# Optimization experiments

Hardware: AMD Instinct MI355X
Metric: run time of the kernel (lower is better)

## Reference

```python
import jax, jax.numpy as jnp
import numpy as np

N_TOKENS, MODEL_DIM, NUM_EXPERTS = 65536, 1024, 64
CAPACITY_FACTOR = 1.0


def setup_inputs() -> dict:
    key = jax.random.key(0)
    k1, k2 = jax.random.split(key)
    x = jax.random.normal(k1, (N_TOKENS, MODEL_DIM), dtype=jnp.float32)
    # gate projection weight, torch Linear stores [out_features, in_features]
    wg = jax.random.normal(k2, (NUM_EXPERTS, MODEL_DIM), dtype=jnp.float32) * (1.0 / np.sqrt(MODEL_DIM))
    return {"x": x, "wg": wg}


def reference(x, wg):
    N, E = x.shape[0], wg.shape[0]
    logits = x @ wg.T                              # [N, E]
    # training-branch capacity: capacity_factor * ceil(N / E)
    capacity = int(CAPACITY_FACTOR * ((N + E - 1) // E))
    indices1_s = jnp.argmax(logits, axis=1)        # [N] top-1 expert per token
    gates = jax.nn.softmax(logits, axis=1)         # [N, E]
    mask1 = jax.nn.one_hot(indices1_s, E, dtype=gates.dtype)  # [N, E]
    gates1_s = jnp.sum(gates * mask1, axis=1)      # [N] gate value of chosen expert
    # locations1_s[i] = number of earlier tokens routed to the same expert
    # (exclusive prefix count = inclusive cumsum - 1 at the selected column)
    locations1 = jnp.cumsum(mask1, axis=0) - 1.0   # [N, E]
    locations1_s = jnp.sum(locations1 * mask1, axis=1).astype(jnp.int32)
    # auxiliary load-balance loss (float32 branch of the original)
    me = jnp.sum(gates, axis=0)                    # [E]
    ce = jnp.sum(mask1, axis=0)                    # [E]
    l_aux = jnp.sum(me * ce) * (E / (N * N))
    return (l_aux, indices1_s.astype(jnp.int32), capacity, locations1_s, gates1_s, E)
```

## Files before the change

kernel.cpp:

```cpp
#include <hip/hip_runtime.h>

#define NT 65536
#define MD 1024
#define NE 64
#define TB 128
#define NGATE (NT / TB)
#define NGRP (NT / 64)

typedef short bf16x8 __attribute__((ext_vector_type(8)));
typedef float f32x4  __attribute__((ext_vector_type(4)));

__device__ __forceinline__ void split1(float f, ushort& h, ushort& m, ushort& lo) {
    unsigned u  = __float_as_uint(f);
    unsigned hb = u & 0xFFFF0000u;
    float    r1 = f - __uint_as_float(hb);
    unsigned mb = __float_as_uint(r1) & 0xFFFF0000u;
    float    r2 = r1 - __uint_as_float(mb);
    h  = (ushort)(hb >> 16);
    m  = (ushort)(mb >> 16);
    lo = (ushort)(__float_as_uint(r2) >> 16);
}

__device__ __forceinline__ void split8(const float4 a, const float4 b,
                                       bf16x8& h, bf16x8& m, bf16x8& lo) {
    float f[8] = {a.x, a.y, a.z, a.w, b.x, b.y, b.z, b.w};
#pragma unroll
    for (int j = 0; j < 8; ++j) {
        ushort hh, mm, ll;
        split1(f[j], hh, mm, ll);
        h[j] = (short)hh; m[j] = (short)mm; lo[j] = (short)ll;
    }
}

__global__ __launch_bounds__(256) void prep_kernel(
    const float* __restrict__ wg, ushort* __restrict__ wgp)
{
    const int idx = blockIdx.x * 256 + threadIdx.x;
    const int l  = idx & 63;
    const int nt = (idx >> 6) & 3;
    const int c  = idx >> 8;
    const int e  = nt * 16 + (l & 15);
    const int k0 = c * 32 + (l >> 4) * 8;
    const float* src = wg + (size_t)e * MD + k0;
    float4 a = *(const float4*)(src);
    float4 b = *(const float4*)(src + 4);
    bf16x8 h, m, lo;
    split8(a, b, h, m, lo);
    *(bf16x8*)(wgp + (size_t)idx * 8)          = h;
    *(bf16x8*)(wgp + 65536 + (size_t)idx * 8)  = m;
    *(bf16x8*)(wgp + 131072 + (size_t)idx * 8) = lo;
}

#define MFMA6(accv, xh, xm, xl, wh, wm, wl)                                        \
    accv = __builtin_amdgcn_mfma_f32_16x16x32_bf16(xh, wh, accv, 0, 0, 0);         \
    accv = __builtin_amdgcn_mfma_f32_16x16x32_bf16(xh, wm, accv, 0, 0, 0);         \
    accv = __builtin_amdgcn_mfma_f32_16x16x32_bf16(xm, wh, accv, 0, 0, 0);         \
    accv = __builtin_amdgcn_mfma_f32_16x16x32_bf16(xm, wm, accv, 0, 0, 0);         \
    accv = __builtin_amdgcn_mfma_f32_16x16x32_bf16(xh, wl, accv, 0, 0, 0);         \
    accv = __builtin_amdgcn_mfma_f32_16x16x32_bf16(xl, wh, accv, 0, 0, 0);

__global__ __launch_bounds__(256, 2) void gate_kernel(
    const float* __restrict__ x, const ushort* __restrict__ wgp,
    float* __restrict__ out, unsigned* __restrict__ packed_ws,
    int* __restrict__ hist_ws, float* __restrict__ me)
{
    __shared__ float lt[TB * 65];
    __shared__ float inv[TB];

    const int tid = threadIdx.x;
    const int wv  = tid >> 6;
    const int l   = tid & 63;
    const int lr  = l & 15;
    const int lg  = l >> 4;
    const int t0  = blockIdx.x * TB + wv * 32;

    const float*  xa0 = x + (size_t)(t0 + lr) * MD + lg * 8;
    const float*  xa1 = xa0 + 16 * MD;
    const ushort* wbh = wgp + (size_t)l * 8;
    const ushort* wbm = wbh + 65536;
    const ushort* wbl = wbh + 131072;

    f32x4 acc[2][4];
#pragma unroll
    for (int mt = 0; mt < 2; ++mt)
#pragma unroll
        for (int nt = 0; nt < 4; ++nt) acc[mt][nt] = f32x4{0.f, 0.f, 0.f, 0.f};

    float4 a00 = *(const float4*)(xa0);
    float4 a01 = *(const float4*)(xa0 + 4);
    float4 a10 = *(const float4*)(xa1);
    float4 a11 = *(const float4*)(xa1 + 4);

#pragma unroll 2
    for (int c = 0; c < 32; ++c) {
        const ushort* ph = wbh + c * 2048;
        const ushort* pm = wbm + c * 2048;
        const ushort* pl = wbl + c * 2048;
        bf16x8 bh[4], bm_[4], bl[4];
#pragma unroll
        for (int nt = 0; nt < 4; ++nt) {
            bh[nt]  = *(const bf16x8*)(ph + nt * 512);
            bm_[nt] = *(const bf16x8*)(pm + nt * 512);
            bl[nt]  = *(const bf16x8*)(pl + nt * 512);
        }
        float4 c00 = a00, c01 = a01, c10 = a10, c11 = a11;
        if (c < 31) {
            const float* xn0 = xa0 + (c + 1) * 32;
            const float* xn1 = xa1 + (c + 1) * 32;
            a00 = *(const float4*)(xn0);
            a01 = *(const float4*)(xn0 + 4);
            a10 = *(const float4*)(xn1);
            a11 = *(const float4*)(xn1 + 4);
        }
        bf16x8 ah0, am0, al0, ah1, am1, al1;
        split8(c00, c01, ah0, am0, al0);
        split8(c10, c11, ah1, am1, al1);
#pragma unroll
        for (int nt = 0; nt < 4; ++nt) {
            MFMA6(acc[0][nt], ah0, am0, al0, bh[nt], bm_[nt], bl[nt]);
            MFMA6(acc[1][nt], ah1, am1, al1, bh[nt], bm_[nt], bl[nt]);
        }
    }

#pragma unroll
    for (int mt = 0; mt < 2; ++mt)
#pragma unroll
        for (int nt = 0; nt < 4; ++nt)
#pragma unroll
            for (int r = 0; r < 4; ++r)
                lt[(wv * 32 + mt * 16 + lg * 4 + r) * 65 + nt * 16 + lr] =
                    acc[mt][nt][r];
    __syncthreads();

    if (tid < 128) {
        const int grp = tid >> 6;
        const int t   = tid & 63;
        float* row = &lt[(grp * 64 + t) * 65];
        float mx = -1e30f; int am = 0;
        for (int e = 0; e < NE; ++e) {
            float v = row[e];
            if (v > mx) { mx = v; am = e; }
        }
        float s = 0.f;
        for (int e = 0; e < NE; ++e) {
            float ev = __expf(row[e] - mx);
            row[e] = ev;
            s += ev;
        }
        float g = 1.0f / s;
        const int gt = blockIdx.x * TB + grp * 64 + t;
        out[1 + gt] = (float)am;
        out[2 + 2 * NT + gt] = g;
        inv[grp * 64 + t] = g;

        const unsigned long long below = (1ull << t) - 1ull;
        int rank = 0, mycnt = 0;
        for (int e = 0; e < NE; ++e) {
            unsigned long long msk = __ballot(am == e);
            if (t == e)  mycnt = (int)__popcll(msk);
            if (am == e) rank  = (int)__popcll(msk & below);
        }
        packed_ws[gt] = (unsigned)am | ((unsigned)rank << 8);
        hist_ws[(blockIdx.x * 2 + grp) * NE + t] = mycnt;
    }
    __syncthreads();

    if (tid < 128) {
        const int grp = tid >> 6;
        const int e   = tid & 63;
        const float* base = &lt[grp * 64 * 65];
        const float* iv   = &inv[grp * 64];
        float s = 0.f;
        for (int t = 0; t < 64; ++t) s += base[t * 65 + e] * iv[t];
        atomicAdd(&me[e], s);
    }
}

__global__ __launch_bounds__(256) void scan_kernel(
    int* __restrict__ hist_ws, float* __restrict__ ce)
{
    const int e = blockIdx.x;
    const int tid = threadIdx.x;
    const int lane = tid & 63, wave = tid >> 6;
    __shared__ int wtot[4];

    int h[4];
#pragma unroll
    for (int j = 0; j < 4; ++j) h[j] = hist_ws[(tid * 4 + j) * NE + e];
    int s = h[0] + h[1] + h[2] + h[3];

    int scan = s;
#pragma unroll
    for (int d = 1; d < 64; d <<= 1) {
        int o = __shfl_up(scan, d, 64);
        if (lane >= d) scan += o;
    }
    if (lane == 63) wtot[wave] = scan;
    __syncthreads();
    int wpre = 0;
#pragma unroll
    for (int w = 0; w < 4; ++w)
        if (w < wave) wpre += wtot[w];

    int run = wpre + scan - s;
#pragma unroll
    for (int j = 0; j < 4; ++j) {
        hist_ws[(tid * 4 + j) * NE + e] = run;
        run += h[j];
    }
    if (tid == 255) ce[e] = (float)run;
}

__global__ __launch_bounds__(256) void emit_kernel(
    const unsigned* __restrict__ packed_ws, const int* __restrict__ offs_ws,
    const float* __restrict__ me, const float* __restrict__ ce,
    float* __restrict__ out)
{
    const int i = blockIdx.x * 256 + threadIdx.x;
    const unsigned p = packed_ws[i];
    const int am = (int)(p & 63u);
    const int rank = (int)(p >> 8);
    const int b = i >> 6;
    out[2 + NT + i] = (float)(offs_ws[b * NE + am] + rank);

    if (blockIdx.x == 0 && threadIdx.x < 64) {
        float v = me[threadIdx.x] * ce[threadIdx.x];
#pragma unroll
        for (int d = 32; d > 0; d >>= 1) v += __shfl_down(v, d, 64);
        if (threadIdx.x == 0) {
            out[0] = v * (float)((double)NE / ((double)NT * (double)NT));
            out[1 + NT] = 1024.0f;
            out[2 + 3 * NT] = 64.0f;
        }
    }
}

extern "C" void kernel_launch(void* const* d_in, const int* in_sizes, int n_in,
                              void* d_out, int out_size, void* d_ws, size_t ws_size,
                              hipStream_t stream)
{
    const float* x  = (const float*)d_in[0];
    const float* wg = (const float*)d_in[1];
    float* out = (float*)d_out;

    unsigned* packed_ws = (unsigned*)d_ws;
    int*      hist_ws   = (int*)((char*)d_ws + 262144);
    float*    me        = (float*)((char*)d_ws + 524288);
    float*    ce        = (float*)((char*)d_ws + 524544);
    ushort*   wgp       = (ushort*)((char*)d_ws + 524800);

    hipMemsetAsync(me, 0, NE * sizeof(float), stream);
    prep_kernel<<<32, 256, 0, stream>>>(wg, wgp);
    gate_kernel<<<NGATE, 256, 0, stream>>>(x, wgp, out, packed_ws, hist_ws, me);
    scan_kernel<<<NE, 256, 0, stream>>>(hist_ws, ce);
    emit_kernel<<<NT / 256, 256, 0, stream>>>(packed_ws, hist_ws, me, ce, out);
}
```

Before: 422.9 us.

## Split gate GEMM K dimension across two wave halves and fold memset into prep

The gate kernel now runs 512 threads per block. Each half of the waves handles half of the K=1024 reduction, and the partial logits are combined through shared memory in two phases. B-fragment loads are interleaved with the MFMAs in a double-buffered pattern, which cuts per-wave register pressure and doubles the number of waves available to hide x-load latency. The separate hipMemsetAsync of the me accumulator is folded into prep_kernel to save a launch. The trade-offs are an extra __syncthreads and a read-modify-write pass over the logit tile in LDS.

```diff
diff --git a/kernel.cpp b/kernel.cpp
--- a/kernel.cpp
+++ b/kernel.cpp
@@ -5,7 +5,6 @@
 #define NE 64
 #define TB 128
 #define NGATE (NT / TB)
-#define NGRP (NT / 64)
 
 typedef short bf16x8 __attribute__((ext_vector_type(8)));
 typedef float f32x4  __attribute__((ext_vector_type(4)));
@@ -33,9 +32,11 @@
 }
 
 __global__ __launch_bounds__(256) void prep_kernel(
-    const float* __restrict__ wg, ushort* __restrict__ wgp)
+    const float* __restrict__ wg, ushort* __restrict__ wgp,
+    float* __restrict__ me)
 {
     const int idx = blockIdx.x * 256 + threadIdx.x;
+    if (blockIdx.x == 0 && threadIdx.x < NE) me[threadIdx.x] = 0.f;
     const int l  = idx & 63;
     const int nt = (idx >> 6) & 3;
     const int c  = idx >> 8;
@@ -59,7 +60,12 @@
     accv = __builtin_amdgcn_mfma_f32_16x16x32_bf16(xh, wl, accv, 0, 0, 0);         \
     accv = __builtin_amdgcn_mfma_f32_16x16x32_bf16(xl, wh, accv, 0, 0, 0);
 
-__global__ __launch_bounds__(256, 2) void gate_kernel(
+#define LDB(dst_h, dst_m, dst_l, nt)                                               \
+    dst_h = *(const bf16x8*)(pb + (nt) * 512);                                     \
+    dst_m = *(const bf16x8*)(pb + 65536 + (nt) * 512);                             \
+    dst_l = *(const bf16x8*)(pb + 131072 + (nt) * 512);
+
+__global__ __launch_bounds__(512, 4) void gate_kernel(
     const float* __restrict__ x, const ushort* __restrict__ wgp,
     float* __restrict__ out, unsigned* __restrict__ packed_ws,
     int* __restrict__ hist_ws, float* __restrict__ me)
@@ -70,15 +76,15 @@
     const int tid = threadIdx.x;
     const int wv  = tid >> 6;
     const int l   = tid & 63;
+    const int g   = wv & 3;
+    const int h   = wv >> 2;
     const int lr  = l & 15;
     const int lg  = l >> 4;
-    const int t0  = blockIdx.x * TB + wv * 32;
-
-    const float*  xa0 = x + (size_t)(t0 + lr) * MD + lg * 8;
-    const float*  xa1 = xa0 + 16 * MD;
-    const ushort* wbh = wgp + (size_t)l * 8;
-    const ushort* wbm = wbh + 65536;
-    const ushort* wbl = wbh + 131072;
+
+    const float* xa0 = x + (size_t)(blockIdx.x * TB + g * 32 + lr) * MD
+                         + h * 512 + lg * 8;
+    const float* xa1 = xa0 + 16 * MD;
+    const ushort* wb = wgp + (size_t)l * 8 + (size_t)h * 16 * 2048;
 
     f32x4 acc[2][4];
 #pragma unroll
@@ -91,20 +97,12 @@
     float4 a10 = *(const float4*)(xa1);
     float4 a11 = *(const float4*)(xa1 + 4);
 
-#pragma unroll 2
-    for (int c = 0; c < 32; ++c) {
-        const ushort* ph = wbh + c * 2048;
-        const ushort* pm = wbm + c * 2048;
-        const ushort* pl = wbl + c * 2048;
-        bf16x8 bh[4], bm_[4], bl[4];
-#pragma unroll
-        for (int nt = 0; nt < 4; ++nt) {
-            bh[nt]  = *(const bf16x8*)(ph + nt * 512);
-            bm_[nt] = *(const bf16x8*)(pm + nt * 512);
-            bl[nt]  = *(const bf16x8*)(pl + nt * 512);
-        }
-        float4 c00 = a00, c01 = a01, c10 = a10, c11 = a11;
-        if (c < 31) {
+    for (int c = 0; c < 16; ++c) {
+        const ushort* pb = wb + c * 2048;
+        bf16x8 ah0, am0, al0, ah1, am1, al1;
+        split8(a00, a01, ah0, am0, al0);
+        split8(a10, a11, ah1, am1, al1);
+        if (c < 15) {
             const float* xn0 = xa0 + (c + 1) * 32;
             const float* xn1 = xa1 + (c + 1) * 32;
             a00 = *(const float4*)(xn0);
@@ -112,24 +110,42 @@
             a10 = *(const float4*)(xn1);
             a11 = *(const float4*)(xn1 + 4);
         }
-        bf16x8 ah0, am0, al0, ah1, am1, al1;
-        split8(c00, c01, ah0, am0, al0);
-        split8(c10, c11, ah1, am1, al1);
-#pragma unroll
-        for (int nt = 0; nt < 4; ++nt) {
-            MFMA6(acc[0][nt], ah0, am0, al0, bh[nt], bm_[nt], bl[nt]);
-            MFMA6(acc[1][nt], ah1, am1, al1, bh[nt], bm_[nt], bl[nt]);
-        }
-    }
-
-#pragma unroll
-    for (int mt = 0; mt < 2; ++mt)
-#pragma unroll
-        for (int nt = 0; nt < 4; ++nt)
-#pragma unroll
-            for (int r = 0; r < 4; ++r)
-                lt[(wv * 32 + mt * 16 + lg * 4 + r) * 65 + nt * 16 + lr] =
-                    acc[mt][nt][r];
+        bf16x8 bhA, bmA, blA, bhB, bmB, blB;
+        LDB(bhA, bmA, blA, 0);
+        LDB(bhB, bmB, blB, 1);
+        MFMA6(acc[0][0], ah0, am0, al0, bhA, bmA, blA);
+        MFMA6(acc[1][0], ah1, am1, al1, bhA, bmA, blA);
+        LDB(bhA, bmA, blA, 2);
+        MFMA6(acc[0][1], ah0, am0, al0, bhB, bmB, blB);
+        MFMA6(acc[1][1], ah1, am1, al1, bhB, bmB, blB);
+        LDB(bhB, bmB, blB, 3);
+        MFMA6(acc[0][2], ah0, am0, al0, bhA, bmA, blA);
+        MFMA6(acc[1][2], ah1, am1, al1, bhA, bmA, blA);
+        MFMA6(acc[0][3], ah0, am0, al0, bhB, bmB, blB);
+        MFMA6(acc[1][3], ah1, am1, al1, bhB, bmB, blB);
+    }
+
+    if (h == 0) {
+#pragma unroll
+        for (int mt = 0; mt < 2; ++mt)
+#pragma unroll
+            for (int nt = 0; nt < 4; ++nt)
+#pragma unroll
+                for (int r = 0; r < 4; ++r)
+                    lt[(g * 32 + mt * 16 + lg * 4 + r) * 65 + nt * 16 + lr] =
+                        acc[mt][nt][r];
+    }
+    __syncthreads();
+    if (h == 1) {
+#pragma unroll
+        for (int mt = 0; mt < 2; ++mt)
+#pragma unroll
+            for (int nt = 0; nt < 4; ++nt)
+#pragma unroll
+                for (int r = 0; r < 4; ++r)
+                    lt[(g * 32 + mt * 16 + lg * 4 + r) * 65 + nt * 16 + lr] +=
+                        acc[mt][nt][r];
+    }
     __syncthreads();
 
     if (tid < 128) {
@@ -147,11 +163,11 @@
             row[e] = ev;
             s += ev;
         }
-        float g = 1.0f / s;
+        float gv = 1.0f / s;
         const int gt = blockIdx.x * TB + grp * 64 + t;
         out[1 + gt] = (float)am;
-        out[2 + 2 * NT + gt] = g;
-        inv[grp * 64 + t] = g;
+        out[2 + 2 * NT + gt] = gv;
+        inv[grp * 64 + t] = gv;
 
         const unsigned long long below = (1ull << t) - 1ull;
         int rank = 0, mycnt = 0;
@@ -249,9 +265,8 @@
     float*    ce        = (float*)((char*)d_ws + 524544);
     ushort*   wgp       = (ushort*)((char*)d_ws + 524800);
 
-    hipMemsetAsync(me, 0, NE * sizeof(float), stream);
-    prep_kernel<<<32, 256, 0, stream>>>(wg, wgp);
-    gate_kernel<<<NGATE, 256, 0, stream>>>(x, wgp, out, packed_ws, hist_ws, me);
+    prep_kernel<<<32, 256, 0, stream>>>(wg, wgp, me);
+    gate_kernel<<<NGATE, 512, 0, stream>>>(x, wgp, out, packed_ws, hist_ws, me);
     scan_kernel<<<NE, 256, 0, stream>>>(hist_ws, ce);
     emit_kernel<<<NT / 256, 256, 0, stream>>>(packed_ws, hist_ws, me, ce, out);
 }
```

After: 399.7 us. -5.5%, faster.
